# Optimization experiments

Measured on AMD Instinct MI355X. Metric: run time of the kernel, lower is better.

The kernel has to match this reference:

```python
import jax, jax.numpy as jnp
import numpy as np

TAU = 2.0       # spikingjelly LIFNode default
V_TH = 1.0      # v_threshold default
ALPHA = 2.0     # surrogate.ATan default alpha

@jax.custom_vjp
def atan_spike(x):
    # Heaviside forward, ATan surrogate gradient backward
    return (x >= 0.0).astype(x.dtype)

def _atan_fwd(x):
    return atan_spike(x), x

def _atan_bwd(x, g):
    return (g * (ALPHA / 2.0) / (1.0 + (jnp.pi / 2.0 * ALPHA * x) ** 2),)

atan_spike.defvjp(_atan_fwd, _atan_bwd)

def lif_scan(cur):
    # cur: [T, ...]; LIF with decay_input=True, hard reset to v_reset=0
    def step(v, c):
        v = v + (c - v) / TAU          # charge with decayed input
        s = atan_spike(v - V_TH)       # fire
        v = (1.0 - s) * v              # hard reset (v_reset = 0)
        return v, s
    v0 = jnp.zeros(cur.shape[1:], cur.dtype)
    _, spikes = jax.lax.scan(step, v0, cur)
    return spikes

def setup_inputs() -> dict:
    key = jax.random.key(0)
    k1, k2 = jax.random.split(key, 2)
    T, B, D = 2048, 32, 512
    x = jax.random.normal(k1, (T, B, D), dtype=jnp.float32)
    W = jax.random.normal(k2, (D, D), dtype=jnp.float32) / np.sqrt(D).astype(np.float32)
    b = jnp.zeros((D,), dtype=jnp.float32)
    return {"x": x, "W": W, "b": b}

def reference(x, W, b):
    # x: [T, B, D]
    xs = jnp.stack([x, jnp.flip(x, axis=0)], axis=2)          # [T, B, 2, D]
    cur = jnp.einsum('tbkd,ed->tbke', xs, W) + b              # Linear (y = x W^T + b)
    s = lif_scan(cur)                                          # [T, B, 2, D] spikes
    return s[:, :, 0, :] + jnp.flip(s[:, :, 1, :], axis=0)    # [T, B, D]
```

## Files before the change

### kernel.cpp

```cpp
#include <hip/hip_runtime.h>
#include <cstddef>
#include <cstdint>

#define T_LEN 2048
#define B_SZ  32
#define D_SZ  512
#define BD    (B_SZ * D_SZ)

#define BM   128
#define BN   128

typedef const __attribute__((address_space(1))) uint32_t* gas1_t;
typedef __attribute__((address_space(3))) uint32_t* las3_t;

__global__ __launch_bounds__(256) void gemm8x8_kernel(
    const float* __restrict__ A,
    const float* __restrict__ W,
    const float* __restrict__ bias,
    float* __restrict__ Y)
{
#pragma clang fp contract(off)
  __shared__ float As[2][BM * 16];
  __shared__ float Bs[2][BN * 16];

  const int tid = threadIdx.x;
  const int tx  = tid & 15;
  const int ty  = tid >> 4;
  const int cA  = ty & 3;
  const int cB  = (tx >> 1) & 3;

  const int nwg  = (int)(gridDim.x * gridDim.y);
  const int orig = (int)(blockIdx.y * gridDim.x + blockIdx.x);
  const int q    = nwg >> 3, r = nwg & 7;
  const int xcd  = orig & 7, loc = orig >> 3;
  const int tix  = (xcd < r ? xcd * (q + 1) : r * (q + 1) + (xcd - r) * q) + loc;
  const int m0   = (tix >> 2) * BM;
  const int n0   = (tix & 3) * BN;

  const int lane  = tid & 63;
  const int wid   = tid >> 6;
  const int rloc  = lane >> 2;
  const int qA4   = (((lane & 3) ^ (rloc & 3)) << 2);
  const int qB4   = (((lane & 3) ^ ((rloc >> 1) & 3)) << 2);
  const int s0    = 2 * wid, s1 = 2 * wid + 1;
  const int oS0   = s0 * 256, oS1 = s1 * 256;
  const float* gA0 = A + (size_t)(m0 + s0 * 16 + rloc) * D_SZ + qA4;
  const float* gA1 = A + (size_t)(m0 + s1 * 16 + rloc) * D_SZ + qA4;
  const float* gB0 = W + (size_t)(n0 + s0 * 16 + rloc) * D_SZ + qB4;
  const float* gB1 = W + (size_t)(n0 + s1 * 16 + rloc) * D_SZ + qB4;

#define STAGE(BUF, KOFF)                                                      \
  do {                                                                        \
    __builtin_amdgcn_global_load_lds((gas1_t)(const void*)(gA0 + (KOFF)),     \
                                     (las3_t)(void*)(&As[BUF][oS0]), 16, 0, 0);\
    __builtin_amdgcn_global_load_lds((gas1_t)(const void*)(gA1 + (KOFF)),     \
                                     (las3_t)(void*)(&As[BUF][oS1]), 16, 0, 0);\
    __builtin_amdgcn_global_load_lds((gas1_t)(const void*)(gB0 + (KOFF)),     \
                                     (las3_t)(void*)(&Bs[BUF][oS0]), 16, 0, 0);\
    __builtin_amdgcn_global_load_lds((gas1_t)(const void*)(gB1 + (KOFF)),     \
                                     (las3_t)(void*)(&Bs[BUF][oS1]), 16, 0, 0);\
  } while (0)

  float acc[8][8];
#pragma unroll
  for (int i = 0; i < 8; ++i)
#pragma unroll
    for (int j = 0; j < 8; ++j) acc[i][j] = 0.0f;

  STAGE(0, 0);
  __syncthreads();

#pragma unroll 1
  for (int kc = 0; kc < 32; ++kc) {
    const int cur = kc & 1;
    if (kc + 1 < 32) STAGE(cur ^ 1, (kc + 1) * 16);

    const float* asb = &As[cur][0];
    const float* bsb = &Bs[cur][0];
#pragma unroll
    for (int kq = 0; kq < 4; ++kq) {
      const int bq = ((kq ^ cB) & 3) << 2;
      const int aq = ((kq ^ cA) & 3) << 2;
      float4 bfr[8];
#pragma unroll
      for (int j = 0; j < 8; ++j)
        bfr[j] = *(const float4*)&bsb[(tx + 16 * j) * 16 + bq];
#pragma unroll
      for (int i = 0; i < 8; ++i) {
        const float4 a = *(const float4*)&asb[(ty + 16 * i) * 16 + aq];
#pragma unroll
        for (int j = 0; j < 8; ++j) {
          acc[i][j] = fmaf(a.x, bfr[j].x, acc[i][j]);
          acc[i][j] = fmaf(a.y, bfr[j].y, acc[i][j]);
          acc[i][j] = fmaf(a.z, bfr[j].z, acc[i][j]);
          acc[i][j] = fmaf(a.w, bfr[j].w, acc[i][j]);
        }
      }
    }
    __syncthreads();
  }
#undef STAGE

#pragma unroll
  for (int i = 0; i < 8; ++i) {
    const int m = m0 + ty + 16 * i;
#pragma unroll
    for (int j = 0; j < 8; ++j) {
      const int n = n0 + tx + 16 * j;
      Y[(size_t)m * D_SZ + n] = acc[i][j] + bias[n];
    }
  }
}

#define CHK   8
#define CLEN  256

__global__ __launch_bounds__(64) void scan_chunk_kernel(
    const float* __restrict__ Y,
    float* __restrict__ out)
{
#pragma clang fp contract(off)
  const int idx = blockIdx.x * 64 + threadIdx.x;
  const int c   = blockIdx.y;
  const int t0  = c * CLEN;
  float ca[32], cb[32];
  uint32_t sf0, sf1, sf2, sf3, sf4, sf5, sf6, sf7;
  float v;

#define LD(R, TB)                                                             \
  _Pragma("unroll")                                                           \
  for (int j = 0; j < 32; ++j) R[j] = Y[(size_t)((TB) + j) * BD + idx];

#define FCH(R, WREC)                                                          \
  {                                                                           \
    uint32_t w_ = 0;                                                          \
    _Pragma("unroll")                                                         \
    for (int j = 0; j < 32; ++j) {                                            \
      v = v + (R[j] - v) * 0.5f;                                              \
      const bool s = (v - 1.0f) >= 0.0f;                                      \
      w_ |= (uint32_t)s << j;                                                 \
      v = s ? 0.0f : v;                                                       \
    }                                                                         \
    WREC;                                                                     \
  }

#define BCH(R, WREC)                                                          \
  {                                                                           \
    uint32_t w_ = 0;                                                          \
    _Pragma("unroll")                                                         \
    for (int j = 31; j >= 0; --j) {                                           \
      v = v + (R[j] - v) * 0.5f;                                              \
      const bool s = (v - 1.0f) >= 0.0f;                                      \
      w_ |= (uint32_t)s << j;                                                 \
      v = s ? 0.0f : v;                                                       \
    }                                                                         \
    WREC;                                                                     \
  }

#define WOUT(SF, G)                                                           \
  _Pragma("unroll")                                                           \
  for (int j = 0; j < 32; ++j)                                                \
    out[(size_t)(t0 + (G) * 32 + j) * BD + idx] =                             \
        (float)(((SF >> j) & 1u) + ((w_ >> j) & 1u));

  v = 0.0f;
  if (c > 0) {
    LD(ca, t0 - 64)
    LD(cb, t0 - 32)
    FCH(ca, (void)0)
    LD(ca, t0)
    FCH(cb, (void)0)
  } else {
    LD(ca, t0)
  }
  LD(cb, t0 + 32)  FCH(ca, sf0 = w_)
  LD(ca, t0 + 64)  FCH(cb, sf1 = w_)
  LD(cb, t0 + 96)  FCH(ca, sf2 = w_)
  LD(ca, t0 + 128) FCH(cb, sf3 = w_)
  LD(cb, t0 + 160) FCH(ca, sf4 = w_)
  LD(ca, t0 + 192) FCH(cb, sf5 = w_)
  LD(cb, t0 + 224) FCH(ca, sf6 = w_)
                   FCH(cb, sf7 = w_)

  v = 0.0f;
  if (c < CHK - 1) {
    LD(ca, t0 + CLEN + 32)
    LD(cb, t0 + CLEN)
    BCH(ca, (void)0)
    LD(ca, t0 + 224)
    BCH(cb, (void)0)
  } else {
    LD(ca, t0 + 224)
  }
  LD(cb, t0 + 192) BCH(ca, WOUT(sf7, 7))
  LD(ca, t0 + 160) BCH(cb, WOUT(sf6, 6))
  LD(cb, t0 + 128) BCH(ca, WOUT(sf5, 5))
  LD(ca, t0 + 96)  BCH(cb, WOUT(sf4, 4))
  LD(cb, t0 + 64)  BCH(ca, WOUT(sf3, 3))
  LD(ca, t0 + 32)  BCH(cb, WOUT(sf2, 2))
  LD(cb, t0)       BCH(ca, WOUT(sf1, 1))
                   BCH(cb, WOUT(sf0, 0))

#undef LD
#undef FCH
#undef BCH
#undef WOUT
}

__global__ __launch_bounds__(64) void lif_fwd_kernel(
    const float* __restrict__ Y, float* __restrict__ out,
    int tlen, float* __restrict__ vstate, int carry)
{
#pragma clang fp contract(off)
  const int idx = blockIdx.x * 64 + threadIdx.x;
  float v = carry ? vstate[idx] : 0.0f;
#pragma unroll 16
  for (int t = 0; t < tlen; ++t) {
    const float c = Y[(size_t)t * BD + idx];
    v = v + (c - v) * 0.5f;
    const bool s = (v - 1.0f) >= 0.0f;
    out[(size_t)t * BD + idx] = s ? 1.0f : 0.0f;
    v = s ? 0.0f : v;
  }
  vstate[idx] = v;
}

__global__ __launch_bounds__(64) void lif_bwd_kernel(
    const float* __restrict__ Y, float* __restrict__ out,
    int tlen, float* __restrict__ vstate, int carry)
{
#pragma clang fp contract(off)
  const int idx = blockIdx.x * 64 + threadIdx.x;
  float v = carry ? vstate[idx] : 0.0f;
#pragma unroll 16
  for (int tt = 0; tt < tlen; ++tt) {
    const size_t t = (size_t)(tlen - 1 - tt);
    const float c = Y[t * BD + idx];
    v = v + (c - v) * 0.5f;
    const bool s = (v - 1.0f) >= 0.0f;
    out[t * BD + idx] += s ? 1.0f : 0.0f;
    v = s ? 0.0f : v;
  }
  vstate[idx] = v;
}

extern "C" void kernel_launch(void* const* d_in, const int* in_sizes, int n_in,
                              void* d_out, int out_size, void* d_ws, size_t ws_size,
                              hipStream_t stream)
{
  const float* x = (const float*)d_in[0];
  const float* W = (const float*)d_in[1];
  const float* b = (const float*)d_in[2];
  float* out = (float*)d_out;

  const size_t full_bytes = (size_t)T_LEN * BD * sizeof(float);
  const size_t vbytes     = (size_t)BD * sizeof(float);

  if (ws_size >= full_bytes) {
    float* Y = (float*)d_ws;
    dim3 grid(T_LEN * B_SZ / BM, D_SZ / BN);
    gemm8x8_kernel<<<grid, 256, 0, stream>>>(x, W, b, Y);
    scan_chunk_kernel<<<dim3(BD / 64, CHK), 64, 0, stream>>>(Y, out);
  } else {
    const size_t avail = ws_size > vbytes ? ws_size - vbytes : 0;
    int Tc = T_LEN;
    while (Tc > 4 && (size_t)Tc * BD * sizeof(float) > avail) Tc >>= 1;
    float* Y      = (float*)d_ws;
    float* vstate = (float*)((char*)d_ws + (size_t)Tc * BD * sizeof(float));

    int first = 1;
    for (int t0 = 0; t0 < T_LEN; t0 += Tc) {
      dim3 grid(Tc * B_SZ / BM, D_SZ / BN);
      gemm8x8_kernel<<<grid, 256, 0, stream>>>(x + (size_t)t0 * BD, W, b, Y);
      lif_fwd_kernel<<<BD / 64, 64, 0, stream>>>(Y, out + (size_t)t0 * BD, Tc,
                                                 vstate, first ? 0 : 1);
      first = 0;
    }
    first = 1;
    for (int t0 = T_LEN - Tc; t0 >= 0; t0 -= Tc) {
      dim3 grid(Tc * B_SZ / BM, D_SZ / BN);
      gemm8x8_kernel<<<grid, 256, 0, stream>>>(x + (size_t)t0 * BD, W, b, Y);
      lif_bwd_kernel<<<BD / 64, 64, 0, stream>>>(Y, out + (size_t)t0 * BD, Tc,
                                                 vstate, first ? 0 : 1);
      first = 0;
    }
  }
}
```

Baseline: 761.2 us.

## Halve scan chunk length, defer spike writes, and simplify GEMM A-tile addressing

The scan kernel now splits time into 16 chunks of 128 steps instead of 8 chunks of 256. This doubles the number of parallel workgroups, at the cost of relatively more 64-step warm-up recomputation per chunk. Backward spike words are now stored in registers and all outputs are written at the end rather than interleaved with the backward pass. The GEMM drops the XOR swizzle on the A tile, loads all eight A float4s up front, and streams B per column, trading possible LDS bank conflicts on A for simpler addressing and a different register schedule.

Result: faster. 676.9 us (-11.1%).

```diff
diff --git a/kernel.cpp b/kernel.cpp
--- a/kernel.cpp
+++ b/kernel.cpp
@@ -26,7 +26,6 @@
   const int tid = threadIdx.x;
   const int tx  = tid & 15;
   const int ty  = tid >> 4;
-  const int cA  = ty & 3;
   const int cB  = (tx >> 1) & 3;
 
   const int nwg  = (int)(gridDim.x * gridDim.y);
@@ -40,7 +39,7 @@
   const int lane  = tid & 63;
   const int wid   = tid >> 6;
   const int rloc  = lane >> 2;
-  const int qA4   = (((lane & 3) ^ (rloc & 3)) << 2);
+  const int qA4   = ((lane & 3) << 2);
   const int qB4   = (((lane & 3) ^ ((rloc >> 1) & 3)) << 2);
   const int s0    = 2 * wid, s1 = 2 * wid + 1;
   const int oS0   = s0 * 256, oS1 = s1 * 256;
@@ -75,26 +74,31 @@
     const int cur = kc & 1;
     if (kc + 1 < 32) STAGE(cur ^ 1, (kc + 1) * 16);
 
-    const float* asb = &As[cur][0];
-    const float* bsb = &Bs[cur][0];
+    const float* asb = &As[cur][0] + ty * 16;
+    const float* bsb = &Bs[cur][0] + tx * 16;
 #pragma unroll
     for (int kq = 0; kq < 4; ++kq) {
+      const int aq = kq << 2;
       const int bq = ((kq ^ cB) & 3) << 2;
-      const int aq = ((kq ^ cA) & 3) << 2;
-      float4 bfr[8];
-#pragma unroll
-      for (int j = 0; j < 8; ++j)
-        bfr[j] = *(const float4*)&bsb[(tx + 16 * j) * 16 + bq];
-#pragma unroll
-      for (int i = 0; i < 8; ++i) {
-        const float4 a = *(const float4*)&asb[(ty + 16 * i) * 16 + aq];
-#pragma unroll
-        for (int j = 0; j < 8; ++j) {
-          acc[i][j] = fmaf(a.x, bfr[j].x, acc[i][j]);
-          acc[i][j] = fmaf(a.y, bfr[j].y, acc[i][j]);
-          acc[i][j] = fmaf(a.z, bfr[j].z, acc[i][j]);
-          acc[i][j] = fmaf(a.w, bfr[j].w, acc[i][j]);
-        }
+      const float4 a0 = *(const float4*)&asb[0 * 256 + aq];
+      const float4 a1 = *(const float4*)&asb[1 * 256 + aq];
+      const float4 a2 = *(const float4*)&asb[2 * 256 + aq];
+      const float4 a3 = *(const float4*)&asb[3 * 256 + aq];
+      const float4 a4 = *(const float4*)&asb[4 * 256 + aq];
+      const float4 a5 = *(const float4*)&asb[5 * 256 + aq];
+      const float4 a6 = *(const float4*)&asb[6 * 256 + aq];
+      const float4 a7 = *(const float4*)&asb[7 * 256 + aq];
+#pragma unroll
+      for (int j = 0; j < 8; ++j) {
+        const float4 b = *(const float4*)&bsb[j * 256 + bq];
+#define FMA4(I, AV)                                                           \
+        acc[I][j] = fmaf(AV.x, b.x, acc[I][j]);                               \
+        acc[I][j] = fmaf(AV.y, b.y, acc[I][j]);                               \
+        acc[I][j] = fmaf(AV.z, b.z, acc[I][j]);                               \
+        acc[I][j] = fmaf(AV.w, b.w, acc[I][j]);
+        FMA4(0, a0) FMA4(1, a1) FMA4(2, a2) FMA4(3, a3)
+        FMA4(4, a4) FMA4(5, a5) FMA4(6, a6) FMA4(7, a7)
+#undef FMA4
       }
     }
     __syncthreads();
@@ -112,8 +116,8 @@
   }
 }
 
-#define CHK   8
-#define CLEN  256
+#define CHK  16
+#define CLEN 128
 
 __global__ __launch_bounds__(64) void scan_chunk_kernel(
     const float* __restrict__ Y,
@@ -124,14 +128,14 @@
   const int c   = blockIdx.y;
   const int t0  = c * CLEN;
   float ca[32], cb[32];
-  uint32_t sf0, sf1, sf2, sf3, sf4, sf5, sf6, sf7;
+  uint32_t sf0, sf1, sf2, sf3, sb0, sb1, sb2, sb3;
   float v;
 
 #define LD(R, TB)                                                             \
   _Pragma("unroll")                                                           \
   for (int j = 0; j < 32; ++j) R[j] = Y[(size_t)((TB) + j) * BD + idx];
 
-#define FCH(R, WREC)                                                          \
+#define FCH(R, W)                                                             \
   {                                                                           \
     uint32_t w_ = 0;                                                          \
     _Pragma("unroll")                                                         \
@@ -141,10 +145,10 @@
       w_ |= (uint32_t)s << j;                                                 \
       v = s ? 0.0f : v;                                                       \
     }                                                                         \
-    WREC;                                                                     \
-  }
-
-#define BCH(R, WREC)                                                          \
+    W = w_;                                                                   \
+  }
+
+#define BCH(R, W)                                                             \
   {                                                                           \
     uint32_t w_ = 0;                                                          \
     _Pragma("unroll")                                                         \
@@ -154,57 +158,52 @@
       w_ |= (uint32_t)s << j;                                                 \
       v = s ? 0.0f : v;                                                       \
     }                                                                         \
-    WREC;                                                                     \
-  }
-
-#define WOUT(SF, G)                                                           \
-  _Pragma("unroll")                                                           \
-  for (int j = 0; j < 32; ++j)                                                \
-    out[(size_t)(t0 + (G) * 32 + j) * BD + idx] =                             \
-        (float)(((SF >> j) & 1u) + ((w_ >> j) & 1u));
+    W = w_;                                                                   \
+  }
+
+  uint32_t wdump;
 
   v = 0.0f;
   if (c > 0) {
     LD(ca, t0 - 64)
     LD(cb, t0 - 32)
-    FCH(ca, (void)0)
+    FCH(ca, wdump)
     LD(ca, t0)
-    FCH(cb, (void)0)
+    FCH(cb, wdump)
   } else {
     LD(ca, t0)
   }
-  LD(cb, t0 + 32)  FCH(ca, sf0 = w_)
-  LD(ca, t0 + 64)  FCH(cb, sf1 = w_)
-  LD(cb, t0 + 96)  FCH(ca, sf2 = w_)
-  LD(ca, t0 + 128) FCH(cb, sf3 = w_)
-  LD(cb, t0 + 160) FCH(ca, sf4 = w_)
-  LD(ca, t0 + 192) FCH(cb, sf5 = w_)
-  LD(cb, t0 + 224) FCH(ca, sf6 = w_)
-                   FCH(cb, sf7 = w_)
+  LD(cb, t0 + 32)  FCH(ca, sf0)
+  LD(ca, t0 + 64)  FCH(cb, sf1)
+  LD(cb, t0 + 96)  FCH(ca, sf2)
+                   FCH(cb, sf3)
 
   v = 0.0f;
   if (c < CHK - 1) {
     LD(ca, t0 + CLEN + 32)
     LD(cb, t0 + CLEN)
-    BCH(ca, (void)0)
-    LD(ca, t0 + 224)
-    BCH(cb, (void)0)
+    BCH(ca, wdump)
+    LD(ca, t0 + 96)
+    BCH(cb, wdump)
   } else {
-    LD(ca, t0 + 224)
-  }
-  LD(cb, t0 + 192) BCH(ca, WOUT(sf7, 7))
-  LD(ca, t0 + 160) BCH(cb, WOUT(sf6, 6))
-  LD(cb, t0 + 128) BCH(ca, WOUT(sf5, 5))
-  LD(ca, t0 + 96)  BCH(cb, WOUT(sf4, 4))
-  LD(cb, t0 + 64)  BCH(ca, WOUT(sf3, 3))
-  LD(ca, t0 + 32)  BCH(cb, WOUT(sf2, 2))
-  LD(cb, t0)       BCH(ca, WOUT(sf1, 1))
-                   BCH(cb, WOUT(sf0, 0))
+    LD(ca, t0 + 96)
+  }
+  LD(cb, t0 + 64)  BCH(ca, sb3)
+  LD(ca, t0 + 32)  BCH(cb, sb2)
+  LD(cb, t0)       BCH(ca, sb1)
+                   BCH(cb, sb0)
+
+#define WGRP(SF, SB, G)                                                       \
+  _Pragma("unroll")                                                           \
+  for (int j = 0; j < 32; ++j)                                                \
+    out[(size_t)(t0 + (G) * 32 + j) * BD + idx] =                             \
+        (float)(((SF >> j) & 1u) + ((SB >> j) & 1u));
+  WGRP(sf0, sb0, 0) WGRP(sf1, sb1, 1) WGRP(sf2, sb2, 2) WGRP(sf3, sb3, 3)
 
 #undef LD
 #undef FCH
 #undef BCH
-#undef WOUT
+#undef WGRP
 }
 
 __global__ __launch_bounds__(64) void lif_fwd_kernel(
```
